# Performance work log

Hardware: AMD Instinct MI355X
Metric: run time of the kernel (lower is better)

The kernel has to match this reference:

```python
import jax, jax.numpy as jnp
import numpy as np

HIDDEN = 1024
HEADS = 16
HEAD_DIM = HIDDEN // HEADS
B, S = 2, 2048


def setup_inputs() -> dict:
    key = jax.random.key(0)
    ks = jax.random.split(key, 11)
    std = 1.0 / np.sqrt(HIDDEN)
    return {
        "query": jax.random.normal(ks[0], (B, S, HIDDEN), dtype=jnp.float32),
        "key": jax.random.normal(ks[1], (B, S, HIDDEN), dtype=jnp.float32),
        "value": jax.random.normal(ks[2], (B, S, HIDDEN), dtype=jnp.float32),
        "Wq": jax.random.uniform(ks[3], (HIDDEN, HIDDEN), jnp.float32, -std, std),
        "bq": jax.random.uniform(ks[4], (HIDDEN,), jnp.float32, -std, std),
        "Wk": jax.random.uniform(ks[5], (HIDDEN, HIDDEN), jnp.float32, -std, std),
        "bk": jax.random.uniform(ks[6], (HIDDEN,), jnp.float32, -std, std),
        "Wv": jax.random.uniform(ks[7], (HIDDEN, HIDDEN), jnp.float32, -std, std),
        "bv": jax.random.uniform(ks[8], (HIDDEN,), jnp.float32, -std, std),
        "Wo": jax.random.uniform(ks[9], (HIDDEN, HIDDEN), jnp.float32, -std, std),
        "bo": jax.random.uniform(ks[10], (HIDDEN,), jnp.float32, -std, std),
    }


def reference(query, key, value, Wq, bq, Wk, bk, Wv, bv, Wo, bo):
    b = query.shape[0]
    scale = jnp.sqrt(jnp.float32(HEAD_DIM))
    # linear projections (torch Linear: x @ W.T + b), split into heads -> [b, h, s, d]
    def proj(x, W, bias):
        y = x @ W.T + bias
        return y.reshape(b, -1, HEADS, HEAD_DIM).transpose(0, 2, 1, 3)
    Q = proj(query, Wq, bq)
    K = proj(key, Wk, bk)
    V = proj(value, Wv, bv)
    scores = jnp.einsum("bhqd,bhkd->bhqk", Q, K) / scale
    attn = jax.nn.softmax(scores, axis=-1)
    ctx = jnp.einsum("bhqk,bhkd->bhqd", attn, V)
    ctx = ctx.transpose(0, 2, 1, 3).reshape(b, -1, HIDDEN)
    return ctx @ Wo.T + bo
```

## Files before the change

### kernel.cpp

```cpp
#include <hip/hip_runtime.h>

typedef __attribute__((ext_vector_type(8))) short short8;
typedef __attribute__((ext_vector_type(4))) float float4_t;
typedef __attribute__((ext_vector_type(16))) float f32x16;
typedef __attribute__((ext_vector_type(4))) unsigned int uint4_t;
typedef __attribute__((ext_vector_type(2))) unsigned int uint2_t;
typedef unsigned short u16;

#define HIDDEN 1024
#define HDIM   64
#define SS     2048
#define TOK    4096
#define QSCALE 0.1803368801111137f

__device__ __forceinline__ unsigned int fbits(float f) {
  unsigned int x; __builtin_memcpy(&x, &f, 4); return x;
}
__device__ __forceinline__ u16 f2bf(float f) {
  return (u16)((fbits(f) + 0x8000u) >> 16);
}
__device__ __forceinline__ unsigned int pk2bf(float a, float b) {
  return __builtin_amdgcn_perm(fbits(b) + 0x8000u, fbits(a) + 0x8000u, 0x07060302);
}
__device__ __forceinline__ unsigned int pk2bf_t(float a, float b) {
  return __builtin_amdgcn_perm(fbits(b), fbits(a), 0x07060302);
}

__device__ __forceinline__ void gl_lds16(const u16* g, u16* l) {
  __builtin_amdgcn_global_load_lds(
      (const __attribute__((address_space(1))) unsigned int*)g,
      (__attribute__((address_space(3))) unsigned int*)l, 16, 0, 0);
}

__global__ __launch_bounds__(256) void convert_all(
    const float* __restrict__ w0, const float* __restrict__ w1,
    const float* __restrict__ w2, const float* __restrict__ w3,
    const float* __restrict__ x0, const float* __restrict__ x1,
    const float* __restrict__ x2, u16* __restrict__ Wall, u16* __restrict__ Xall) {
  int y = blockIdx.y;
  const float* src; u16* dst;
  if (y < 4) {
    if (blockIdx.x >= 512) return;
    src = y == 0 ? w0 : y == 1 ? w1 : y == 2 ? w2 : w3;
    dst = Wall + ((size_t)y << 20);
  } else {
    src = y == 4 ? x0 : y == 5 ? x1 : x2;
    dst = Xall + ((size_t)(y - 4) << 22);
  }
  int g = (blockIdx.x * 256 + threadIdx.x) * 8;
  float4_t a = *(const float4_t*)(src + g);
  float4_t b = *(const float4_t*)(src + g + 4);
  uint4_t o;
  o.x = pk2bf(a[0], a[1]); o.y = pk2bf(a[2], a[3]);
  o.z = pk2bf(b[0], b[1]); o.w = pk2bf(b[2], b[3]);
  *(uint4_t*)(dst + g) = o;
}

template<int MTILES, bool AXF32, bool OUTF32>
__device__ __forceinline__ void gemm_bt_body(
    const void* __restrict__ X, const u16* __restrict__ Wb,
    const float* __restrict__ bias, void* __restrict__ Y, int mode, float oscale,
    u16* sA, u16* sB, int row0, int col0) {
  const int tid  = threadIdx.x;
  const int wv   = tid >> 6, lane = tid & 63, quad = lane >> 4, ln = lane & 15;
  const int wm   = (wv >> 1) * (MTILES * 16), wn = (wv & 1) * 64;
  constexpr int AITERS = MTILES;

  float4_t acc[MTILES][4];
#pragma unroll
  for (int i = 0; i < MTILES; i++)
#pragma unroll
    for (int j = 0; j < 4; j++) acc[i][j] = (float4_t)0.0f;

  for (int kt = 0; kt < 16; ++kt) {
    const int k0 = kt * 64;
    short8 ax[AITERS];
    if (AXF32) {
#pragma unroll
      for (int i = 0; i < AITERS; i++) {
        int idx = i * 256 + tid, r = idx >> 3, c = idx & 7;
        const float* p = (const float*)X + (size_t)(row0 + r) * HIDDEN + k0 + c * 8;
        float4_t a = *(const float4_t*)p;
        float4_t b = *(const float4_t*)(p + 4);
        union { unsigned int u[4]; short8 s; } x;
        x.u[0] = pk2bf(a[0], a[1]); x.u[1] = pk2bf(a[2], a[3]);
        x.u[2] = pk2bf(b[0], b[1]); x.u[3] = pk2bf(b[2], b[3]);
        ax[i] = x.s;
      }
    }
    __syncthreads();
#pragma unroll
    for (int i = 0; i < 4; i++) {
      int idx = i * 256 + tid, r = idx >> 3, c = idx & 7;
      int gc = c ^ (r & 7);
      gl_lds16(Wb + (size_t)(col0 + r) * HIDDEN + k0 + gc * 8, sB + idx * 8);
    }
    if (AXF32) {
#pragma unroll
      for (int i = 0; i < AITERS; i++) {
        int idx = i * 256 + tid, r = idx >> 3, c = idx & 7;
        int pos = c ^ (r & 7);
        *(short8*)(sA + r * 64 + pos * 8) = ax[i];
      }
    } else {
#pragma unroll
      for (int i = 0; i < AITERS; i++) {
        int idx = i * 256 + tid, r = idx >> 3, c = idx & 7;
        int gc = c ^ (r & 7);
        gl_lds16((const u16*)X + (size_t)(row0 + r) * HIDDEN + k0 + gc * 8, sA + idx * 8);
      }
    }
    __syncthreads();

    short8 af[MTILES][2], bfr[4][2];
#pragma unroll
    for (int mt = 0; mt < MTILES; mt++)
#pragma unroll
      for (int kk = 0; kk < 2; kk++) {
        int r = wm + mt * 16 + ln;
        int ch = kk * 4 + quad;
        af[mt][kk] = *(const short8*)(sA + r * 64 + (ch ^ (r & 7)) * 8);
      }
#pragma unroll
    for (int nt = 0; nt < 4; nt++)
#pragma unroll
      for (int kk = 0; kk < 2; kk++) {
        int r = wn + nt * 16 + ln;
        int ch = kk * 4 + quad;
        bfr[nt][kk] = *(const short8*)(sB + r * 64 + (ch ^ (r & 7)) * 8);
      }
#pragma unroll
    for (int kk = 0; kk < 2; kk++)
#pragma unroll
      for (int mt = 0; mt < MTILES; mt++)
#pragma unroll
        for (int nt = 0; nt < 4; nt++)
          acc[mt][nt] = __builtin_amdgcn_mfma_f32_16x16x32_bf16(af[mt][kk], bfr[nt][kk], acc[mt][nt], 0, 0, 0);
  }

  float bcol[4];
#pragma unroll
  for (int nt = 0; nt < 4; nt++) bcol[nt] = bias[col0 + wn + nt * 16 + ln];
#pragma unroll
  for (int mt = 0; mt < MTILES; mt++)
#pragma unroll
    for (int nt = 0; nt < 4; nt++) {
      int n = col0 + wn + nt * 16 + ln;
#pragma unroll
      for (int r = 0; r < 4; r++) {
        int m = row0 + wm + mt * 16 + quad * 4 + r;
        float v = (acc[mt][nt][r] + bcol[nt]) * oscale;
        if (mode == 0) {
          if (OUTF32) ((float*)Y)[(size_t)m * HIDDEN + n] = v;
          else        ((u16*)Y)[(size_t)m * HIDDEN + n] = f2bf(v);
        } else {
          ((u16*)Y)[((size_t)(m >> 11) * HIDDEN + n) * SS + (m & 2047)] = f2bf(v);
        }
      }
    }
}

__global__ __launch_bounds__(256) void qkv_gemm_bf16(
    const u16* __restrict__ Xall, const u16* __restrict__ Wall,
    const float* __restrict__ bq, const float* __restrict__ bk, const float* __restrict__ bv,
    u16* __restrict__ Qp, u16* __restrict__ Kp, u16* __restrict__ Vt) {
  __shared__ u16 sA[128 * 64];
  __shared__ u16 sB[128 * 64];
  int z = blockIdx.z;
  const u16* X = Xall + ((size_t)z << 22);
  const u16* W = Wall + ((size_t)z << 20);
  const float* Bp = z == 0 ? bq : z == 1 ? bk : bv;
  u16* Y = z == 0 ? Qp : z == 1 ? Kp : Vt;
  int mode = (z == 2) ? 1 : 0;
  float sc = (z == 0) ? QSCALE : 1.0f;
  gemm_bt_body<4, false, false>(X, W, Bp, Y, mode, sc, sA, sB, blockIdx.y * 128, blockIdx.x * 128);
}

__global__ __launch_bounds__(256) void qkv_gemm_f32(
    const float* __restrict__ xq, const float* __restrict__ xk, const float* __restrict__ xv,
    const u16* __restrict__ Wall,
    const float* __restrict__ bq, const float* __restrict__ bk, const float* __restrict__ bv,
    u16* __restrict__ Qp, u16* __restrict__ Kp, u16* __restrict__ Vt) {
  __shared__ u16 sA[128 * 64];
  __shared__ u16 sB[128 * 64];
  int z = blockIdx.z;
  const float* X = z == 0 ? xq : z == 1 ? xk : xv;
  const u16* W = Wall + ((size_t)z << 20);
  const float* Bp = z == 0 ? bq : z == 1 ? bk : bv;
  u16* Y = z == 0 ? Qp : z == 1 ? Kp : Vt;
  int mode = (z == 2) ? 1 : 0;
  float sc = (z == 0) ? QSCALE : 1.0f;
  gemm_bt_body<4, true, false>(X, W, Bp, Y, mode, sc, sA, sB, blockIdx.y * 128, blockIdx.x * 128);
}

__global__ __launch_bounds__(256) void out_gemm(
    const u16* __restrict__ X, const u16* __restrict__ Wob,
    const float* __restrict__ bias, float* __restrict__ Y) {
  __shared__ u16 sA[64 * 64];
  __shared__ u16 sB[128 * 64];
  gemm_bt_body<2, false, true>(X, Wob, bias, Y, 0, 1.0f, sA, sB, blockIdx.y * 64, blockIdx.x * 128);
}

__global__ __launch_bounds__(256, 1) void attn(
    const u16* __restrict__ Qp, const u16* __restrict__ Kp,
    const u16* __restrict__ Vt, u16* __restrict__ Ctx) {
  __shared__ u16 sK[2][128 * 64];
  __shared__ u16 sV[2][64 * 128];
  const int tid  = threadIdx.x;
  const int wv   = tid >> 6, lane = tid & 63;
  const int l5   = lane >> 5, ln = lane & 31;
  const int f = blockIdx.x;
  const int qt = f >> 5, g = f & 31, h = g >> 1, b = g & 1;
  const int row0w = qt * 256 + wv * 64;

  short8 qf[2][4];
#pragma unroll
  for (int qg = 0; qg < 2; ++qg)
#pragma unroll
    for (int kk = 0; kk < 4; ++kk)
      qf[qg][kk] = *(const short8*)(Qp + (size_t)(b * SS + row0w + qg * 32 + ln) * HIDDEN
                                    + h * HDIM + kk * 16 + l5 * 8);

  f32x16 oacc[2][2];
#pragma unroll
  for (int qg = 0; qg < 2; ++qg)
#pragma unroll
    for (int dg = 0; dg < 2; ++dg) oacc[qg][dg] = (f32x16)0.0f;
  float dsum[2] = {0.f, 0.f};

  auto stage = [&](int buf, int kt) {
#pragma unroll
    for (int p = 0; p < 4; ++p) {
      int off = p * 256 + tid;
      { int r = off >> 3, c = off & 7;  int gc = c ^ (r & 7);
        gl_lds16(Kp + (size_t)(b * SS + kt * 128 + r) * HIDDEN + h * HDIM + gc * 8,
                 &sK[buf][0] + off * 8); }
      { int r = off >> 4, c = off & 15; int gc = c ^ (r & 15);
        gl_lds16(Vt + ((size_t)b * HIDDEN + h * HDIM + r) * SS + kt * 128 + gc * 8,
                 &sV[buf][0] + off * 8); }
    }
  };

  stage(0, 0);
  __syncthreads();

  for (int kt = 0; kt < 16; ++kt) {
    const int cur = kt & 1;
    if (kt < 15) stage(cur ^ 1, kt + 1);
    const u16* K_ = &sK[cur][0];
    const u16* V_ = &sV[cur][0];

#pragma unroll
    for (int kgg = 0; kgg < 4; ++kgg) {
      f32x16 st[2];
      st[0] = (f32x16)0.0f; st[1] = (f32x16)0.0f;
#pragma unroll
      for (int kk = 0; kk < 4; ++kk) {
        int r = kgg * 32 + ln;
        int ch = kk * 2 + l5;
        short8 kf = *(const short8*)(K_ + r * 64 + ((ch ^ (r & 7))) * 8);
        st[0] = __builtin_amdgcn_mfma_f32_32x32x16_bf16(kf, qf[0][kk], st[0], 0, 0, 0);
        st[1] = __builtin_amdgcn_mfma_f32_32x32x16_bf16(kf, qf[1][kk], st[1], 0, 0, 0);
      }

      union PF { unsigned int u[4]; short8 s; };
      PF pfr[2][2];
#pragma unroll
      for (int qg = 0; qg < 2; ++qg) {
        float p[16];
#pragma unroll
        for (int r = 0; r < 16; ++r)
          p[r] = __builtin_amdgcn_exp2f(fminf(st[qg][r], 80.f));
        dsum[qg] += (((p[0] + p[1]) + (p[2] + p[3])) + ((p[4] + p[5]) + (p[6] + p[7])))
                  + (((p[8] + p[9]) + (p[10] + p[11])) + ((p[12] + p[13]) + (p[14] + p[15])));
        unsigned int pk[8];
#pragma unroll
        for (int i = 0; i < 8; ++i) pk[i] = pk2bf_t(p[2 * i], p[2 * i + 1]);
        uint2_t r02 = __builtin_amdgcn_permlane32_swap(pk[0], pk[2], false, false);
        uint2_t r13 = __builtin_amdgcn_permlane32_swap(pk[1], pk[3], false, false);
        uint2_t r46 = __builtin_amdgcn_permlane32_swap(pk[4], pk[6], false, false);
        uint2_t r57 = __builtin_amdgcn_permlane32_swap(pk[5], pk[7], false, false);
        pfr[qg][0].u[0] = r02.x; pfr[qg][0].u[1] = r13.x;
        pfr[qg][0].u[2] = r02.y; pfr[qg][0].u[3] = r13.y;
        pfr[qg][1].u[0] = r46.x; pfr[qg][1].u[1] = r57.x;
        pfr[qg][1].u[2] = r46.y; pfr[qg][1].u[3] = r57.y;
      }

#pragma unroll
      for (int ks = 0; ks < 2; ++ks) {
        int ch = (kgg * 2 + ks) * 2 + l5;
#pragma unroll
        for (int dg = 0; dg < 2; ++dg) {
          int r = dg * 32 + ln;
          short8 vf = *(const short8*)(V_ + r * 128 + ((ch ^ (r & 15))) * 8);
          oacc[0][dg] = __builtin_amdgcn_mfma_f32_32x32x16_bf16(vf, pfr[0][ks].s, oacc[0][dg], 0, 0, 0);
          oacc[1][dg] = __builtin_amdgcn_mfma_f32_32x32x16_bf16(vf, pfr[1][ks].s, oacc[1][dg], 0, 0, 0);
        }
      }
    }
    __syncthreads();
  }

  float inv[2];
#pragma unroll
  for (int qg = 0; qg < 2; ++qg) {
    float s = dsum[qg] + __shfl_xor(dsum[qg], 32, 64);
    inv[qg] = 1.0f / s;
  }

  u16* ep = ((u16*)sK) + wv * 4096;
#pragma unroll
  for (int qg = 0; qg < 2; ++qg) {
    int row = qg * 32 + ln;
#pragma unroll
    for (int dg = 0; dg < 2; ++dg)
#pragma unroll
      for (int i = 0; i < 4; ++i) {
        uint2_t w;
        w.x = pk2bf(oacc[qg][dg][4 * i] * inv[qg],     oacc[qg][dg][4 * i + 1] * inv[qg]);
        w.y = pk2bf(oacc[qg][dg][4 * i + 2] * inv[qg], oacc[qg][dg][4 * i + 3] * inv[qg]);
        int c = dg * 4 + i;
        *(uint2_t*)(ep + row * 64 + ((c ^ (row & 7))) * 8 + l5 * 4) = w;
      }
  }
#pragma unroll
  for (int ps = 0; ps < 8; ++ps) {
    int r = ps * 8 + (lane >> 3);
    int c = lane & 7;
    short8 o8 = *(const short8*)(ep + r * 64 + ((c ^ (r & 7))) * 8);
    *(short8*)(Ctx + (size_t)(b * SS + row0w + r) * HIDDEN + h * HDIM + c * 8) = o8;
  }
}

extern "C" void kernel_launch(void* const* d_in, const int* in_sizes, int n_in,
                              void* d_out, int out_size, void* d_ws, size_t ws_size,
                              hipStream_t stream) {
  const float* q  = (const float*)d_in[0];
  const float* k  = (const float*)d_in[1];
  const float* v  = (const float*)d_in[2];
  const float* Wq = (const float*)d_in[3];
  const float* bq = (const float*)d_in[4];
  const float* Wk = (const float*)d_in[5];
  const float* bk = (const float*)d_in[6];
  const float* Wv = (const float*)d_in[7];
  const float* bv = (const float*)d_in[8];
  const float* Wo = (const float*)d_in[9];
  const float* bo = (const float*)d_in[10];

  u16* Qp   = (u16*)d_ws;
  u16* Kp   = Qp + (size_t)TOK * HIDDEN;
  u16* Vt   = Kp + (size_t)TOK * HIDDEN;
  u16* Wall = Vt + (size_t)TOK * HIDDEN;
  u16* Xall = Wall + (4u << 20);
  u16* Cx   = Qp;
  bool useX = ws_size >= (size_t)56 * 1024 * 1024;

  dim3 blk(256);
  if (useX) {
    hipLaunchKernelGGL(convert_all, dim3(2048, 7), blk, 0, stream,
                       Wq, Wk, Wv, Wo, q, k, v, Wall, Xall);
    hipLaunchKernelGGL(qkv_gemm_bf16, dim3(8, 32, 3), blk, 0, stream,
                       Xall, Wall, bq, bk, bv, Qp, Kp, Vt);
  } else {
    hipLaunchKernelGGL(convert_all, dim3(512, 4), blk, 0, stream,
                       Wq, Wk, Wv, Wo, q, k, v, Wall, Wall);
    hipLaunchKernelGGL(qkv_gemm_f32, dim3(8, 32, 3), blk, 0, stream,
                       q, k, v, Wall, bq, bk, bv, Qp, Kp, Vt);
  }
  hipLaunchKernelGGL(attn, dim3(256), blk, 0, stream, Qp, Kp, Vt, Cx);
  hipLaunchKernelGGL(out_gemm, dim3(8, 64, 1), blk, 0, stream,
                     Cx, Wall + (3u << 20), bo, (float*)d_out);
}
```

Before: 243.3 us.

## Halve attention query tile per wave to double block count and occupancy

```diff
diff --git a/kernel.cpp b/kernel.cpp
--- a/kernel.cpp
+++ b/kernel.cpp
@@ -201,7 +201,7 @@
   gemm_bt_body<2, false, true>(X, Wob, bias, Y, 0, 1.0f, sA, sB, blockIdx.y * 64, blockIdx.x * 128);
 }
 
-__global__ __launch_bounds__(256, 1) void attn(
+__global__ __launch_bounds__(256, 2) void attn(
     const u16* __restrict__ Qp, const u16* __restrict__ Kp,
     const u16* __restrict__ Vt, u16* __restrict__ Ctx) {
   __shared__ u16 sK[2][128 * 64];
@@ -211,22 +211,17 @@
   const int l5   = lane >> 5, ln = lane & 31;
   const int f = blockIdx.x;
   const int qt = f >> 5, g = f & 31, h = g >> 1, b = g & 1;
-  const int row0w = qt * 256 + wv * 64;
-
-  short8 qf[2][4];
-#pragma unroll
-  for (int qg = 0; qg < 2; ++qg)
-#pragma unroll
-    for (int kk = 0; kk < 4; ++kk)
-      qf[qg][kk] = *(const short8*)(Qp + (size_t)(b * SS + row0w + qg * 32 + ln) * HIDDEN
-                                    + h * HDIM + kk * 16 + l5 * 8);
-
-  f32x16 oacc[2][2];
-#pragma unroll
-  for (int qg = 0; qg < 2; ++qg)
-#pragma unroll
-    for (int dg = 0; dg < 2; ++dg) oacc[qg][dg] = (f32x16)0.0f;
-  float dsum[2] = {0.f, 0.f};
+  const int row0w = qt * 128 + wv * 32;
+
+  short8 qf[4];
+#pragma unroll
+  for (int kk = 0; kk < 4; ++kk)
+    qf[kk] = *(const short8*)(Qp + (size_t)(b * SS + row0w + ln) * HIDDEN
+                              + h * HDIM + kk * 16 + l5 * 8);
+
+  f32x16 oacc[2];
+  oacc[0] = (f32x16)0.0f; oacc[1] = (f32x16)0.0f;
+  float dsum = 0.f;
 
   auto stage = [&](int buf, int kt) {
 #pragma unroll
@@ -252,27 +247,24 @@
 
 #pragma unroll
     for (int kgg = 0; kgg < 4; ++kgg) {
-      f32x16 st[2];
-      st[0] = (f32x16)0.0f; st[1] = (f32x16)0.0f;
+      f32x16 st = (f32x16)0.0f;
 #pragma unroll
       for (int kk = 0; kk < 4; ++kk) {
         int r = kgg * 32 + ln;
         int ch = kk * 2 + l5;
         short8 kf = *(const short8*)(K_ + r * 64 + ((ch ^ (r & 7))) * 8);
-        st[0] = __builtin_amdgcn_mfma_f32_32x32x16_bf16(kf, qf[0][kk], st[0], 0, 0, 0);
-        st[1] = __builtin_amdgcn_mfma_f32_32x32x16_bf16(kf, qf[1][kk], st[1], 0, 0, 0);
+        st = __builtin_amdgcn_mfma_f32_32x32x16_bf16(kf, qf[kk], st, 0, 0, 0);
       }
 
       union PF { unsigned int u[4]; short8 s; };
-      PF pfr[2][2];
-#pragma unroll
-      for (int qg = 0; qg < 2; ++qg) {
+      PF pfr[2];
+      {
         float p[16];
 #pragma unroll
         for (int r = 0; r < 16; ++r)
-          p[r] = __builtin_amdgcn_exp2f(fminf(st[qg][r], 80.f));
-        dsum[qg] += (((p[0] + p[1]) + (p[2] + p[3])) + ((p[4] + p[5]) + (p[6] + p[7])))
-                  + (((p[8] + p[9]) + (p[10] + p[11])) + ((p[12] + p[13]) + (p[14] + p[15])));
+          p[r] = __builtin_amdgcn_exp2f(fminf(st[r], 80.f));
+        dsum += (((p[0] + p[1]) + (p[2] + p[3])) + ((p[4] + p[5]) + (p[6] + p[7])))
+              + (((p[8] + p[9]) + (p[10] + p[11])) + ((p[12] + p[13]) + (p[14] + p[15])));
         unsigned int pk[8];
 #pragma unroll
         for (int i = 0; i < 8; ++i) pk[i] = pk2bf_t(p[2 * i], p[2 * i + 1]);
@@ -280,10 +272,10 @@
         uint2_t r13 = __builtin_amdgcn_permlane32_swap(pk[1], pk[3], false, false);
         uint2_t r46 = __builtin_amdgcn_permlane32_swap(pk[4], pk[6], false, false);
         uint2_t r57 = __builtin_amdgcn_permlane32_swap(pk[5], pk[7], false, false);
-        pfr[qg][0].u[0] = r02.x; pfr[qg][0].u[1] = r13.x;
-        pfr[qg][0].u[2] = r02.y; pfr[qg][0].u[3] = r13.y;
-        pfr[qg][1].u[0] = r46.x; pfr[qg][1].u[1] = r57.x;
-        pfr[qg][1].u[2] = r46.y; pfr[qg][1].u[3] = r57.y;
+        pfr[0].u[0] = r02.x; pfr[0].u[1] = r13.x;
+        pfr[0].u[2] = r02.y; pfr[0].u[3] = r13.y;
+        pfr[1].u[0] = r46.x; pfr[1].u[1] = r57.x;
+        pfr[1].u[2] = r46.y; pfr[1].u[3] = r57.y;
       }
 
 #pragma unroll
@@ -293,38 +285,32 @@
         for (int dg = 0; dg < 2; ++dg) {
           int r = dg * 32 + ln;
           short8 vf = *(const short8*)(V_ + r * 128 + ((ch ^ (r & 15))) * 8);
-          oacc[0][dg] = __builtin_amdgcn_mfma_f32_32x32x16_bf16(vf, pfr[0][ks].s, oacc[0][dg], 0, 0, 0);
-          oacc[1][dg] = __builtin_amdgcn_mfma_f32_32x32x16_bf16(vf, pfr[1][ks].s, oacc[1][dg], 0, 0, 0);
+          oacc[dg] = __builtin_amdgcn_mfma_f32_32x32x16_bf16(vf, pfr[ks].s, oacc[dg], 0, 0, 0);
         }
       }
     }
     __syncthreads();
   }
 
-  float inv[2];
-#pragma unroll
-  for (int qg = 0; qg < 2; ++qg) {
-    float s = dsum[qg] + __shfl_xor(dsum[qg], 32, 64);
-    inv[qg] = 1.0f / s;
-  }
-
-  u16* ep = ((u16*)sK) + wv * 4096;
-#pragma unroll
-  for (int qg = 0; qg < 2; ++qg) {
-    int row = qg * 32 + ln;
+  float s = dsum + __shfl_xor(dsum, 32, 64);
+  float inv = 1.0f / s;
+
+  u16* ep = ((u16*)sK) + wv * 2048;
+  {
+    int row = ln;
 #pragma unroll
     for (int dg = 0; dg < 2; ++dg)
 #pragma unroll
       for (int i = 0; i < 4; ++i) {
         uint2_t w;
-        w.x = pk2bf(oacc[qg][dg][4 * i] * inv[qg],     oacc[qg][dg][4 * i + 1] * inv[qg]);
-        w.y = pk2bf(oacc[qg][dg][4 * i + 2] * inv[qg], oacc[qg][dg][4 * i + 3] * inv[qg]);
+        w.x = pk2bf(oacc[dg][4 * i] * inv,     oacc[dg][4 * i + 1] * inv);
+        w.y = pk2bf(oacc[dg][4 * i + 2] * inv, oacc[dg][4 * i + 3] * inv);
         int c = dg * 4 + i;
         *(uint2_t*)(ep + row * 64 + ((c ^ (row & 7))) * 8 + l5 * 4) = w;
       }
   }
 #pragma unroll
-  for (int ps = 0; ps < 8; ++ps) {
+  for (int ps = 0; ps < 4; ++ps) {
     int r = ps * 8 + (lane >> 3);
     int c = lane & 7;
     short8 o8 = *(const short8*)(ep + r * 64 + ((c ^ (r & 7))) * 8);
@@ -367,7 +353,7 @@
     hipLaunchKernelGGL(qkv_gemm_f32, dim3(8, 32, 3), blk, 0, stream,
                        q, k, v, Wall, bq, bk, bv, Qp, Kp, Vt);
   }
-  hipLaunchKernelGGL(attn, dim3(256), blk, 0, stream, Qp, Kp, Vt, Cx);
+  hipLaunchKernelGGL(attn, dim3(512), blk, 0, stream, Qp, Kp, Vt, Cx);
   hipLaunchKernelGGL(out_gemm, dim3(8, 64, 1), blk, 0, stream,
                      Cx, Wall + (3u << 20), bo, (float*)d_out);
 }
```

After: 213.8 us. 1.14x faster.
